# Optimization experiments

Measured on AMD Instinct MI355X. Metric: run time of the kernel, lower is better.

## Reference

```python
import jax, jax.numpy as jnp
import numpy as np

B, T, D = 1, 4096, 2048
NUM_HEADS, NUM_KV_HEADS, HEAD_DIM = 16, 8, 128
QUERY_PRE_ATTN_SCALAR = HEAD_DIM ** -0.5
SOFT_CAP = 50.0
WINDOW = 1024
ROPE_BASE = 10000.0
ROPE_SCALE = 1.0
K_MASK = -2.3819763e+38


def apply_rope(x, positions, head_dim, max_wavelength=ROPE_BASE, scale_factor=ROPE_SCALE):
    # x: [B, T, N, H], positions: [B, T]
    fraction = 2.0 * jnp.arange(head_dim // 2, dtype=jnp.float32) / head_dim
    timescale = max_wavelength ** fraction  # [H/2]
    sinusoid = positions[..., None].astype(jnp.float32) / timescale  # [B, T, H/2]
    sinusoid = (sinusoid / scale_factor)[..., None, :]  # [B, T, 1, H/2]
    sin, cos = jnp.sin(sinusoid), jnp.cos(sinusoid)
    first, second = jnp.split(x, 2, axis=-1)
    out = jnp.concatenate([first * cos - second * sin,
                           second * cos + first * sin], axis=-1)
    return out.astype(x.dtype)


def setup_inputs() -> dict:
    key = jax.random.key(0)
    ks = jax.random.split(key, 4)
    x = jax.random.normal(ks[0], (B, T, D), dtype=jnp.float32)
    segment_pos = jnp.broadcast_to(jnp.arange(T, dtype=jnp.int32), (B, T))
    # causal mask [B, T, S]
    attn_mask = jnp.broadcast_to(
        jnp.tril(jnp.ones((T, T), dtype=jnp.bool_)), (B, T, T))
    q_w = jax.random.normal(ks[1], (NUM_HEADS, D, HEAD_DIM), dtype=jnp.float32) * 0.02
    kv_w = jax.random.normal(ks[2], (2, NUM_KV_HEADS, D, HEAD_DIM), dtype=jnp.float32) * 0.02
    o_w = jax.random.normal(ks[3], (NUM_HEADS, HEAD_DIM, D), dtype=jnp.float32) * 0.02
    return {"x": x, "segment_pos": segment_pos, "attn_mask": attn_mask,
            "q_w": q_w, "kv_w": kv_w, "o_w": o_w}


def reference(x, segment_pos, attn_mask, q_w, kv_w, o_w):
    # Projections (GQA: separate q and kv einsums)
    q = jnp.einsum('BTD,NDH->BTNH', x, q_w)          # [B,T,N,H]
    k = jnp.einsum('BSD,KDH->BSKH', x, kv_w[0])      # [B,S,K,H]
    v = jnp.einsum('BSD,KDH->BSKH', x, kv_w[1])      # [B,S,K,H]

    q = apply_rope(q, segment_pos, HEAD_DIM)
    q = q * QUERY_PRE_ATTN_SCALAR
    k = apply_rope(k, segment_pos, HEAD_DIM)

    num_groups = NUM_HEADS // NUM_KV_HEADS
    qg = q.reshape(B, T, NUM_KV_HEADS, num_groups, HEAD_DIM)
    logits = jnp.einsum('BTKGH,BSKH->BTKGS', qg, k)
    logits = logits.reshape(B, T, NUM_HEADS, -1)     # [B,T,N,S]

    # soft cap
    logits = jnp.tanh(logits / SOFT_CAP) * SOFT_CAP

    # sliding-window mask combined with causal mask
    all_ones = jnp.ones_like(attn_mask)
    sliding = jnp.triu(all_ones, -WINDOW + 1) * jnp.tril(all_ones, WINDOW - 1)
    mask = sliding * attn_mask                       # [B,T,S] bool

    padded = jnp.where(mask[:, :, None, :], logits, K_MASK)
    probs = jax.nn.softmax(padded, axis=-1).astype(k.dtype)

    probs_g = probs.reshape(B, T, NUM_KV_HEADS, num_groups, -1)
    encoded = jnp.einsum('BTKGS,BSKH->BTKGH', probs_g, v)
    encoded = encoded.reshape(B, T, NUM_HEADS, HEAD_DIM)

    attn_output = jnp.einsum('BTNH,NHD->BTD', encoded, o_w)
    return attn_output
```

## Files before the change

kernel.cpp:

```cpp
#include <hip/hip_runtime.h>
#include <hip/hip_bf16.h>
#include <math.h>

typedef __attribute__((ext_vector_type(8))) short short8;
typedef __attribute__((ext_vector_type(8))) unsigned short ushort8;
typedef __attribute__((ext_vector_type(4))) float f32x4;

#define T_SEQ 4096
#define D_MODEL 2048
#define N_HEADS 16
#define N_KV 8
#define HEAD_DIM 128
#define QSCALE 0.08838834764831845f

__device__ __forceinline__ float bf2f(unsigned short u) {
  union { unsigned int i; float f; } x; x.i = ((unsigned int)u) << 16; return x.f;
}
__device__ __forceinline__ unsigned short f2bf(float f) {
  union { float f; unsigned int i; } x; x.f = f;
  unsigned int i = x.i;
  unsigned int r = i + 0x7fffu + ((i >> 16) & 1u);
  return (unsigned short)(r >> 16);
}

__global__ __launch_bounds__(256) void cvt_x_kernel(const float* __restrict__ x,
                                                    unsigned short* __restrict__ xb) {
  int idx = blockIdx.x * 256 + threadIdx.x;
  const float4* p = reinterpret_cast<const float4*>(x) + (size_t)idx * 2;
  float4 a = p[0], b = p[1];
  ushort8 o;
  o[0] = f2bf(a.x); o[1] = f2bf(a.y); o[2] = f2bf(a.z); o[3] = f2bf(a.w);
  o[4] = f2bf(b.x); o[5] = f2bf(b.y); o[6] = f2bf(b.z); o[7] = f2bf(b.w);
  reinterpret_cast<ushort8*>(xb)[idx] = o;
}

__global__ __launch_bounds__(256) void rope_table_kernel(const int* __restrict__ segpos,
                                                         float2* __restrict__ tab) {
  int idx = blockIdx.x * 256 + threadIdx.x;
  int t = idx >> 6, i = idx & 63;
  float pos = (float)segpos[t];
  float ts = powf(10000.f, (float)(2 * i) / 128.f);
  float ang = pos / ts;
  tab[idx] = make_float2(sinf(ang), cosf(ang));
}

__global__ __launch_bounds__(256) void transpose_f32_bf16_kernel(const float* __restrict__ src,
                                                                 unsigned short* __restrict__ dst,
                                                                 int sstride, int dstride,
                                                                 long sBatch, long dBatch) {
  __shared__ float tile[32][33];
  long b = blockIdx.z;
  src += b * sBatch; dst += b * dBatch;
  int c0 = blockIdx.x * 32, r0 = blockIdx.y * 32;
  int tx = threadIdx.x & 31, ty = threadIdx.x >> 5;
#pragma unroll
  for (int i = 0; i < 4; ++i)
    tile[ty + i * 8][tx] = src[(size_t)(r0 + ty + i * 8) * sstride + c0 + tx];
  __syncthreads();
#pragma unroll
  for (int i = 0; i < 4; ++i)
    dst[(size_t)(c0 + ty + i * 8) * dstride + r0 + tx] = f2bf(tile[tx][ty + i * 8]);
}

__global__ __launch_bounds__(256) void transpose_bf16_kernel(const unsigned short* __restrict__ src,
                                                             unsigned short* __restrict__ dst,
                                                             int sstride, int dstride,
                                                             long sBatch, long dBatch) {
  __shared__ unsigned short tile[32][33];
  long b = blockIdx.z;
  src += b * sBatch; dst += b * dBatch;
  int c0 = blockIdx.x * 32, r0 = blockIdx.y * 32;
  int tx = threadIdx.x & 31, ty = threadIdx.x >> 5;
#pragma unroll
  for (int i = 0; i < 4; ++i)
    tile[ty + i * 8][tx] = src[(size_t)(r0 + ty + i * 8) * sstride + c0 + tx];
  __syncthreads();
#pragma unroll
  for (int i = 0; i < 4; ++i)
    dst[(size_t)(c0 + ty + i * 8) * dstride + r0 + tx] = tile[tx][ty + i * 8];
}

#define G2L(gp, lp)                                                           \
  __builtin_amdgcn_global_load_lds(                                           \
      (const __attribute__((address_space(1))) void*)(gp),                    \
      (__attribute__((address_space(3))) void*)(lp), 16, 0, 0)
#define GBAR() asm volatile("s_barrier" ::: "memory")
#define VMW(n) asm volatile("s_waitcnt vmcnt(" #n ")" ::: "memory")

template <int OUT_BF16, int NHB>
__global__ __launch_bounds__(512, 2) void gemm256_kernel(const unsigned short* __restrict__ A,
                                                         const unsigned short* __restrict__ Bt,
                                                         void* __restrict__ Cout,
                                                         int M, int N, int K) {
  constexpr int NW = 2 * NHB;
  extern __shared__ unsigned short smem[];
  unsigned short* ldsA = smem;
  unsigned short* ldsB = smem + 32768;
  const int tid = threadIdx.x;
  const int lane = tid & 63, wave = tid >> 6;
  const int wm = wave >> 2, wn = wave & 3;
  const int lr = lane & 15, lg = lane >> 4;
  const int swz = (lr & 7) << 3;
  const int c0s = (lg * 8) ^ swz;
  const int c1s = (32 + lg * 8) ^ swz;

  int id = blockIdx.y * gridDim.x + blockIdx.x;
  int nb = gridDim.x * gridDim.y;
  int sw = (id & 7) * (nb >> 3) + (id >> 3);
  const long brow = (long)(sw / gridDim.x) * 256;
  const long bcol = (long)(sw % gridDim.x) * (128 * NHB);

  const unsigned short* Ag = A + brow * K;
  const unsigned short* Bg = Bt + bcol * K;

  const int r0 = tid >> 3;
  const int cs = ((tid & 7) * 8) ^ ((r0 & 7) << 3);

#define ST_A(tt, b, a)                                                        \
  { G2L(Ag + (size_t)((a) * 128 + r0) * K + (size_t)(tt) * 64 + cs,           \
        ldsA + (b) * 16384 + (a) * 8192 + tid * 8);                           \
    G2L(Ag + (size_t)((a) * 128 + r0 + 64) * K + (size_t)(tt) * 64 + cs,      \
        ldsA + (b) * 16384 + (a) * 8192 + 4096 + tid * 8); }
#define ST_B(tt, b, h)                                                        \
  { G2L(Bg + (size_t)((h) * 128 + r0) * K + (size_t)(tt) * 64 + cs,           \
        ldsB + (b) * 8192 * NHB + (h) * 8192 + tid * 8);                      \
    G2L(Bg + (size_t)((h) * 128 + r0 + 64) * K + (size_t)(tt) * 64 + cs,      \
        ldsB + (b) * 8192 * NHB + (h) * 8192 + 4096 + tid * 8); }

  f32x4 acc[8][NW] = {};
  short8 bf[NW][2];
  short8 af[4];

#define RD_B(b)                                                               \
  { const unsigned short* pb = ldsB + (b) * 8192 * NHB + wn * 2048 * NHB;     \
    _Pragma("unroll")                                                         \
    for (int n = 0; n < NW; ++n) {                                            \
      bf[n][0] = *(const short8*)(pb + (n * 16 + lr) * 64 + c0s);             \
      bf[n][1] = *(const short8*)(pb + (n * 16 + lr) * 64 + c1s);             \
    } }
#define RD_A(b, mb)                                                           \
  { const unsigned short* pa = ldsA + (b) * 16384 + wm * 8192;                \
    af[0] = *(const short8*)(pa + ((mb) * 16 + lr) * 64 + c0s);               \
    af[1] = *(const short8*)(pa + ((mb) * 16 + lr) * 64 + c1s);               \
    af[2] = *(const short8*)(pa + ((mb) * 16 + 16 + lr) * 64 + c0s);          \
    af[3] = *(const short8*)(pa + ((mb) * 16 + 16 + lr) * 64 + c1s); }
#define MFMA2(mb)                                                             \
  { __builtin_amdgcn_s_setprio(1);                                            \
    _Pragma("unroll")                                                         \
    for (int n = 0; n < NW; ++n) {                                            \
      acc[mb][n]     = __builtin_amdgcn_mfma_f32_16x16x32_bf16(af[0], bf[n][0], acc[mb][n], 0, 0, 0);     \
      acc[mb][n]     = __builtin_amdgcn_mfma_f32_16x16x32_bf16(af[1], bf[n][1], acc[mb][n], 0, 0, 0);     \
      acc[mb + 1][n] = __builtin_amdgcn_mfma_f32_16x16x32_bf16(af[2], bf[n][0], acc[mb + 1][n], 0, 0, 0); \
      acc[mb + 1][n] = __builtin_amdgcn_mfma_f32_16x16x32_bf16(af[3], bf[n][1], acc[mb + 1][n], 0, 0, 0); \
    }                                                                         \
    __builtin_amdgcn_s_setprio(0); }

  ST_B(0, 0, 0);
  if constexpr (NHB == 2) ST_B(0, 0, 1);
  ST_A(0, 0, 0); ST_A(0, 0, 1);
  ST_B(1, 1, 0);
  if constexpr (NHB == 2) ST_B(1, 1, 1);
  if constexpr (NHB == 2) { VMW(4); } else { VMW(2); }
  ST_A(1, 1, 0); ST_A(1, 1, 1);
  GBAR();

  const int NT = K >> 6;
  for (int j = 0; j < (NT >> 1); ++j) {
    const int t2 = 2 * j + 2, t3 = 2 * j + 3;
    const bool s2 = t2 < NT, s3 = t3 < NT;
    RD_B(0); RD_A(0, 0);
    if (s2) ST_B(t2, 0, 0);
    GBAR(); MFMA2(0); GBAR();
    RD_A(0, 2);
    if constexpr (NHB == 2) { if (s2) ST_B(t2, 0, 1); }
    GBAR(); MFMA2(2); GBAR();
    RD_A(0, 4);
    GBAR(); MFMA2(4); GBAR();
    RD_A(0, 6);
    if (s2) {
      if constexpr (NHB == 2) { VMW(4); } else { VMW(2); }
      ST_A(t2, 0, 0); ST_A(t2, 0, 1);
    } else { VMW(0); }
    GBAR(); MFMA2(6); GBAR();
    RD_B(1); RD_A(1, 0);
    if (s3) ST_B(t3, 1, 0);
    GBAR(); MFMA2(0); GBAR();
    RD_A(1, 2);
    if constexpr (NHB == 2) { if (s3) ST_B(t3, 1, 1); }
    GBAR(); MFMA2(2); GBAR();
    RD_A(1, 4);
    GBAR(); MFMA2(4); GBAR();
    RD_A(1, 6);
    if (s3) {
      if constexpr (NHB == 2) { VMW(4); } else { VMW(2); }
      ST_A(t3, 1, 0); ST_A(t3, 1, 1);
    } else { VMW(0); }
    GBAR(); MFMA2(6); GBAR();
  }

#undef ST_A
#undef ST_B
#undef RD_A
#undef RD_B
#undef MFMA2

#pragma unroll
  for (int m = 0; m < 8; ++m) {
#pragma unroll
    for (int i = 0; i < 4; ++i) {
      long row = brow + wm * 128 + m * 16 + lg * 4 + i;
#pragma unroll
      for (int n = 0; n < NW; ++n) {
        long col = bcol + wn * (32 * NHB) + n * 16 + lr;
        if (OUT_BF16)
          ((unsigned short*)Cout)[row * N + col] = f2bf(acc[m][n][i]);
        else
          ((float*)Cout)[row * N + col] = acc[m][n][i];
      }
    }
  }
}

__global__ __launch_bounds__(256) void rope_apply_kernel(const unsigned short* __restrict__ raw,
                                                         const float2* __restrict__ tab,
                                                         unsigned short* __restrict__ Qb,
                                                         unsigned short* __restrict__ Kb) {
  int gid = blockIdx.x * 256 + threadIdx.x;
  int j = gid & 7;
  int rem = gid >> 3;
  int hs = rem % 24;
  int t = rem / 24;
  int i0 = j * 8;
  float sv[8], cv[8];
  const float2* tp = tab + t * 64 + i0;
#pragma unroll
  for (int q = 0; q < 8; ++q) { float2 sc2 = tp[q]; sv[q] = sc2.x; cv[q] = sc2.y; }
  if (hs < 16) {
    const unsigned short* p = raw + (size_t)t * 4096 + hs * 128 + i0;
    ushort8 a = *(const ushort8*)p;
    ushort8 b = *(const ushort8*)(p + 64);
    ushort8 o1, o2;
#pragma unroll
    for (int q = 0; q < 8; ++q) {
      float fa = bf2f(a[q]), fb = bf2f(b[q]);
      o1[q] = f2bf((fa * cv[q] - fb * sv[q]) * QSCALE);
      o2[q] = f2bf((fb * cv[q] + fa * sv[q]) * QSCALE);
    }
    unsigned short* qp = Qb + ((size_t)hs * T_SEQ + t) * 128 + i0;
    *(ushort8*)qp = o1;
    *(ushort8*)(qp + 64) = o2;
  } else {
    int kn = hs - 16;
    const unsigned short* p = raw + (size_t)t * 4096 + 2048 + kn * 128 + i0;
    ushort8 a = *(const ushort8*)p;
    ushort8 b = *(const ushort8*)(p + 64);
    ushort8 o1, o2;
#pragma unroll
    for (int q = 0; q < 8; ++q) {
      float fa = bf2f(a[q]), fb = bf2f(b[q]);
      o1[q] = f2bf(fa * cv[q] - fb * sv[q]);
      o2[q] = f2bf(fb * cv[q] + fa * sv[q]);
    }
    unsigned short* kp = Kb + ((size_t)kn * T_SEQ + t) * 128 + i0;
    *(ushort8*)kp = o1;
    *(ushort8*)(kp + 64) = o2;
  }
}

__global__ __launch_bounds__(512) void attn_kernel(const unsigned short* __restrict__ Qb,
                                                   const unsigned short* __restrict__ Kb,
                                                   const unsigned short* __restrict__ Vt,
                                                   unsigned short* __restrict__ enc) {
  __shared__ unsigned short Ks[64][128];
  __shared__ unsigned short Vs[128][64];
  __shared__ unsigned short Ps[8][16][72];
  int lin = blockIdx.y * 32 + blockIdx.x;
  lin = (lin & 7) * 64 + (lin >> 3);
  const int h = lin >> 5;
  const int qb0 = (lin & 31) * 128;
  const int kvh = h >> 1;
  const int tid = threadIdx.x, lane = tid & 63, wave = tid >> 6;
  const int qw = qb0 + wave * 16;
  const int lr = lane & 15, lg = lane >> 4;
  const int sw = (lr & 7) << 3;

  short8 aq[4];
  {
    const unsigned short* qp = Qb + ((size_t)h * T_SEQ + qw + lr) * 128 + lg * 8;
#pragma unroll
    for (int c = 0; c < 4; ++c) aq[c] = *(const short8*)(qp + c * 32);
  }
  f32x4 acc[8] = {};
  float lsum = 0.f;

  const int s_lo = (qb0 - 1023) > 0 ? (qb0 - 1023) : 0;
  const int kb_lo = s_lo >> 6, kb_hi = (qb0 + 127) >> 6;

  const int rK = tid >> 4;
  const int cpK = (tid & 15) * 8;
  const int colK = cpK ^ ((rK & 7) << 3);
  const int rV = tid >> 3;
  const int cpV = (tid & 7) * 8;
  const int colV = cpV ^ ((rV & 7) << 3);
  const unsigned short* kgb = Kb + ((size_t)kvh * T_SEQ + rK) * 128 + colK;
  const unsigned short* vgb = Vt + ((size_t)kvh * 128 + rV) * T_SEQ + colV;

  ushort8 kr0, kr1, vr0, vr1;
  {
    const int s0g = kb_lo * 64;
    kr0 = *(const ushort8*)(kgb + (size_t)s0g * 128);
    kr1 = *(const ushort8*)(kgb + (size_t)(s0g + 32) * 128);
    vr0 = *(const ushort8*)(vgb + s0g);
    vr1 = *(const ushort8*)(vgb + (size_t)64 * T_SEQ + s0g);
  }

  const int qg = qw + lr;
  for (int kb = kb_lo; kb <= kb_hi; ++kb) {
    const int s0g = kb * 64;
    __syncthreads();
    *(ushort8*)&Ks[rK][cpK] = kr0;
    *(ushort8*)&Ks[rK + 32][cpK] = kr1;
    *(ushort8*)&Vs[rV][cpV] = vr0;
    *(ushort8*)&Vs[rV + 64][cpV] = vr1;
    __syncthreads();
    if (kb < kb_hi) {
      const int sn = s0g + 64;
      kr0 = *(const ushort8*)(kgb + (size_t)sn * 128);
      kr1 = *(const ushort8*)(kgb + (size_t)(sn + 32) * 128);
      vr0 = *(const ushort8*)(vgb + sn);
      vr1 = *(const ushort8*)(vgb + (size_t)64 * T_SEQ + sn);
    }
    if (s0g > qw + 15 || s0g + 63 < qw - 1023) continue;
    const bool interior = (s0g + 63 <= qw) && (s0g >= qw - 1008);

    f32x4 sT[4] = {};
#pragma unroll
    for (int st = 0; st < 4; ++st) {
      const int krow = st * 16 + lr;
#pragma unroll
      for (int c = 0; c < 4; ++c) {
        short8 kf = *(const short8*)&Ks[krow][(c * 32 + lg * 8) ^ sw];
        sT[st] = __builtin_amdgcn_mfma_f32_16x16x32_bf16(kf, aq[c], sT[st], 0, 0, 0);
      }
    }
#pragma unroll
    for (int st = 0; st < 4; ++st) {
      float p[4];
#pragma unroll
      for (int r = 0; r < 4; ++r) {
        float s = sT[st][r];
        float z2 = s * s * 4.0e-4f;
        float capped = s * (15.f + z2) * __builtin_amdgcn_rcpf(fmaf(z2, 6.f, 15.f));
        float pv = __expf(capped);
        if (!interior) {
          int sg = s0g + st * 16 + lg * 4 + r;
          pv = ((unsigned)(qg - sg) <= 1023u) ? pv : 0.f;
        }
        lsum += pv;
        p[r] = pv;
      }
      unsigned u0, u1;
      asm("v_cvt_pk_bf16_f32 %0, %1, %2" : "=v"(u0) : "v"(p[0]), "v"(p[1]));
      asm("v_cvt_pk_bf16_f32 %0, %1, %2" : "=v"(u1) : "v"(p[2]), "v"(p[3]));
      uint2 w; w.x = u0; w.y = u1;
      *(uint2*)&Ps[wave][lr][st * 16 + lg * 4] = w;
    }
    short8 pa0 = *(const short8*)&Ps[wave][lr][lg * 8];
    short8 pa1 = *(const short8*)&Ps[wave][lr][32 + lg * 8];
#pragma unroll
    for (int d0 = 0; d0 < 8; ++d0) {
      const int vrow = d0 * 16 + lr;
      short8 bv0 = *(const short8*)&Vs[vrow][(lg * 8) ^ sw];
      short8 bv1 = *(const short8*)&Vs[vrow][(32 + lg * 8) ^ sw];
      acc[d0] = __builtin_amdgcn_mfma_f32_16x16x32_bf16(pa0, bv0, acc[d0], 0, 0, 0);
      acc[d0] = __builtin_amdgcn_mfma_f32_16x16x32_bf16(pa1, bv1, acc[d0], 0, 0, 0);
    }
  }

  float l = lsum;
  l += __shfl_xor(l, 16);
  l += __shfl_xor(l, 32);
#pragma unroll
  for (int r = 0; r < 4; ++r) {
    float lt = __shfl(l, lg * 4 + r);
    float inv = __builtin_amdgcn_rcpf(lt);
    int row = qw + lg * 4 + r;
    unsigned short* op = enc + (size_t)row * D_MODEL + h * 128 + lr;
#pragma unroll
    for (int d0 = 0; d0 < 8; ++d0) op[d0 * 16] = f2bf(acc[d0][r] * inv);
  }
}

extern "C" void kernel_launch(void* const* d_in, const int* in_sizes, int n_in,
                              void* d_out, int out_size, void* d_ws, size_t ws_size,
                              hipStream_t stream) {
  const float* x = (const float*)d_in[0];
  const int* segpos = (const int*)d_in[1];
  const float* q_w = (const float*)d_in[3];
  const float* kv_w = (const float*)d_in[4];
  const float* o_w = (const float*)d_in[5];
  float* out = (float*)d_out;
  char* ws = (char*)d_ws;

  const size_t OFF_XB = 0;
  const size_t OFF_WT = OFF_XB + 16777216;
  const size_t OFF_RAW = OFF_WT + 16777216;
  const size_t OFF_KB = OFF_RAW + 33554432;
  const size_t OFF_VT = OFF_KB + 8388608;
  const size_t OFF_TAB = OFF_VT + 8388608;
  unsigned short* xb = (unsigned short*)(ws + OFF_XB);
  unsigned short* Wt = (unsigned short*)(ws + OFF_WT);
  unsigned short* raw = (unsigned short*)(ws + OFF_RAW);
  unsigned short* Kb = (unsigned short*)(ws + OFF_KB);
  unsigned short* Vt = (unsigned short*)(ws + OFF_VT);
  float2* tab = (float2*)(ws + OFF_TAB);
  unsigned short* o_wt = xb;
  unsigned short* Qb = Wt;
  unsigned short* enc = raw;

  hipFuncSetAttribute((const void*)(gemm256_kernel<1, 2>),
                      hipFuncAttributeMaxDynamicSharedMemorySize, 131072);
  hipFuncSetAttribute((const void*)(gemm256_kernel<0, 1>),
                      hipFuncAttributeMaxDynamicSharedMemorySize, 98304);

  cvt_x_kernel<<<dim3(4096), dim3(256), 0, stream>>>(x, xb);
  rope_table_kernel<<<dim3(1024), dim3(256), 0, stream>>>(segpos, tab);
  transpose_f32_bf16_kernel<<<dim3(4, 64, 16), dim3(256), 0, stream>>>(
      q_w, Wt, 128, 2048, (long)2048 * 128, (long)128 * 2048);
  transpose_f32_bf16_kernel<<<dim3(4, 64, 16), dim3(256), 0, stream>>>(
      kv_w, Wt + (size_t)2048 * 2048, 128, 2048, (long)2048 * 128, (long)128 * 2048);
  gemm256_kernel<1, 2><<<dim3(16, 16), dim3(512), 131072, stream>>>(xb, Wt, (void*)raw, 4096, 4096, 2048);
  transpose_f32_bf16_kernel<<<dim3(64, 64, 1), dim3(256), 0, stream>>>(
      o_w, o_wt, 2048, 2048, 0L, 0L);
  rope_apply_kernel<<<dim3(3072), dim3(256), 0, stream>>>(raw, tab, Qb, Kb);
  transpose_bf16_kernel<<<dim3(4, 128, 8), dim3(256), 0, stream>>>(
      raw + 3072, Vt, 4096, 4096, 128L, (long)128 * 4096);
  attn_kernel<<<dim3(32, 16), dim3(512), 0, stream>>>(Qb, Kb, Vt, enc);
  gemm256_kernel<0, 1><<<dim3(16, 16), dim3(512), 98304, stream>>>(enc, o_wt, (void*)out, 4096, 2048, 2048);
}
```

Before: 205.0 us.

## Merge prep kernels, shrink attention blocks to 64 queries, use exp2 and setprio

Several unrelated changes are bundled. The x conversion and rope-table kernels become one launch, the q/kv weight transposes become one launch, and rope application is fused with the V transpose, cutting the launch count. The attention kernel moves from 128-query, 8-wave blocks to 64-query, 4-wave blocks with 1024 blocks in total, and K/V register prefetch is adjusted to match. The softmax folds log2(e) into the soft-cap and masks with -inf before a raw v_exp_f32, and s_setprio is raised around the MFMA sections. Smaller blocks give more blocks per CU, but each block reloads K/V tiles shared across fewer queries, which increases K/V traffic.

```diff
diff --git a/kernel.cpp b/kernel.cpp
--- a/kernel.cpp
+++ b/kernel.cpp
@@ -23,61 +23,60 @@
   return (unsigned short)(r >> 16);
 }
 
-__global__ __launch_bounds__(256) void cvt_x_kernel(const float* __restrict__ x,
-                                                    unsigned short* __restrict__ xb) {
-  int idx = blockIdx.x * 256 + threadIdx.x;
-  const float4* p = reinterpret_cast<const float4*>(x) + (size_t)idx * 2;
-  float4 a = p[0], b = p[1];
-  ushort8 o;
-  o[0] = f2bf(a.x); o[1] = f2bf(a.y); o[2] = f2bf(a.z); o[3] = f2bf(a.w);
-  o[4] = f2bf(b.x); o[5] = f2bf(b.y); o[6] = f2bf(b.z); o[7] = f2bf(b.w);
-  reinterpret_cast<ushort8*>(xb)[idx] = o;
-}
-
-__global__ __launch_bounds__(256) void rope_table_kernel(const int* __restrict__ segpos,
-                                                         float2* __restrict__ tab) {
-  int idx = blockIdx.x * 256 + threadIdx.x;
-  int t = idx >> 6, i = idx & 63;
-  float pos = (float)segpos[t];
-  float ts = powf(10000.f, (float)(2 * i) / 128.f);
-  float ang = pos / ts;
-  tab[idx] = make_float2(sinf(ang), cosf(ang));
-}
-
-__global__ __launch_bounds__(256) void transpose_f32_bf16_kernel(const float* __restrict__ src,
-                                                                 unsigned short* __restrict__ dst,
-                                                                 int sstride, int dstride,
-                                                                 long sBatch, long dBatch) {
+__global__ __launch_bounds__(256) void prep_kernel(const float* __restrict__ x,
+                                                   unsigned short* __restrict__ xb,
+                                                   const int* __restrict__ segpos,
+                                                   float2* __restrict__ tab) {
+  int b = blockIdx.x;
+  if (b < 4096) {
+    int idx = b * 256 + threadIdx.x;
+    const float4* p = reinterpret_cast<const float4*>(x) + (size_t)idx * 2;
+    float4 a = p[0], c = p[1];
+    ushort8 o;
+    o[0] = f2bf(a.x); o[1] = f2bf(a.y); o[2] = f2bf(a.z); o[3] = f2bf(a.w);
+    o[4] = f2bf(c.x); o[5] = f2bf(c.y); o[6] = f2bf(c.z); o[7] = f2bf(c.w);
+    reinterpret_cast<ushort8*>(xb)[idx] = o;
+  } else {
+    int idx = (b - 4096) * 256 + threadIdx.x;
+    int t = idx >> 6, i = idx & 63;
+    float pos = (float)segpos[t];
+    float ts = powf(10000.f, (float)(2 * i) / 128.f);
+    float ang = pos / ts;
+    tab[idx] = make_float2(sinf(ang), cosf(ang));
+  }
+}
+
+__global__ __launch_bounds__(256) void wqkv_transpose_kernel(const float* __restrict__ q_w,
+                                                             const float* __restrict__ kv_w,
+                                                             unsigned short* __restrict__ Wt) {
   __shared__ float tile[32][33];
-  long b = blockIdx.z;
-  src += b * sBatch; dst += b * dBatch;
+  int z = blockIdx.z;
+  const float* src = (z < 16) ? q_w + (size_t)z * 2048 * 128
+                              : kv_w + (size_t)(z - 16) * 2048 * 128;
+  unsigned short* dst = Wt + (size_t)z * 128 * 2048;
   int c0 = blockIdx.x * 32, r0 = blockIdx.y * 32;
   int tx = threadIdx.x & 31, ty = threadIdx.x >> 5;
 #pragma unroll
   for (int i = 0; i < 4; ++i)
-    tile[ty + i * 8][tx] = src[(size_t)(r0 + ty + i * 8) * sstride + c0 + tx];
+    tile[ty + i * 8][tx] = src[(size_t)(r0 + ty + i * 8) * 128 + c0 + tx];
   __syncthreads();
 #pragma unroll
   for (int i = 0; i < 4; ++i)
-    dst[(size_t)(c0 + ty + i * 8) * dstride + r0 + tx] = f2bf(tile[tx][ty + i * 8]);
-}
-
-__global__ __launch_bounds__(256) void transpose_bf16_kernel(const unsigned short* __restrict__ src,
-                                                             unsigned short* __restrict__ dst,
-                                                             int sstride, int dstride,
-                                                             long sBatch, long dBatch) {
-  __shared__ unsigned short tile[32][33];
-  long b = blockIdx.z;
-  src += b * sBatch; dst += b * dBatch;
+    dst[(size_t)(c0 + ty + i * 8) * 2048 + r0 + tx] = f2bf(tile[tx][ty + i * 8]);
+}
+
+__global__ __launch_bounds__(256) void ow_transpose_kernel(const float* __restrict__ src,
+                                                           unsigned short* __restrict__ dst) {
+  __shared__ float tile[32][33];
   int c0 = blockIdx.x * 32, r0 = blockIdx.y * 32;
   int tx = threadIdx.x & 31, ty = threadIdx.x >> 5;
 #pragma unroll
   for (int i = 0; i < 4; ++i)
-    tile[ty + i * 8][tx] = src[(size_t)(r0 + ty + i * 8) * sstride + c0 + tx];
+    tile[ty + i * 8][tx] = src[(size_t)(r0 + ty + i * 8) * 2048 + c0 + tx];
   __syncthreads();
 #pragma unroll
   for (int i = 0; i < 4; ++i)
-    dst[(size_t)(c0 + ty + i * 8) * dstride + r0 + tx] = tile[tx][ty + i * 8];
+    dst[(size_t)(c0 + ty + i * 8) * 2048 + r0 + tx] = f2bf(tile[tx][ty + i * 8]);
 }
 
 #define G2L(gp, lp)                                                           \
@@ -221,63 +220,82 @@
   }
 }
 
-__global__ __launch_bounds__(256) void rope_apply_kernel(const unsigned short* __restrict__ raw,
-                                                         const float2* __restrict__ tab,
-                                                         unsigned short* __restrict__ Qb,
-                                                         unsigned short* __restrict__ Kb) {
-  int gid = blockIdx.x * 256 + threadIdx.x;
-  int j = gid & 7;
-  int rem = gid >> 3;
-  int hs = rem % 24;
-  int t = rem / 24;
-  int i0 = j * 8;
-  float sv[8], cv[8];
-  const float2* tp = tab + t * 64 + i0;
-#pragma unroll
-  for (int q = 0; q < 8; ++q) { float2 sc2 = tp[q]; sv[q] = sc2.x; cv[q] = sc2.y; }
-  if (hs < 16) {
-    const unsigned short* p = raw + (size_t)t * 4096 + hs * 128 + i0;
-    ushort8 a = *(const ushort8*)p;
-    ushort8 b = *(const ushort8*)(p + 64);
-    ushort8 o1, o2;
-#pragma unroll
-    for (int q = 0; q < 8; ++q) {
-      float fa = bf2f(a[q]), fb = bf2f(b[q]);
-      o1[q] = f2bf((fa * cv[q] - fb * sv[q]) * QSCALE);
-      o2[q] = f2bf((fb * cv[q] + fa * sv[q]) * QSCALE);
-    }
-    unsigned short* qp = Qb + ((size_t)hs * T_SEQ + t) * 128 + i0;
-    *(ushort8*)qp = o1;
-    *(ushort8*)(qp + 64) = o2;
+__global__ __launch_bounds__(256) void rope_vt_kernel(const unsigned short* __restrict__ raw,
+                                                      const float2* __restrict__ tab,
+                                                      unsigned short* __restrict__ Qb,
+                                                      unsigned short* __restrict__ Kb,
+                                                      unsigned short* __restrict__ Vt) {
+  __shared__ unsigned short tile[32][33];
+  int b = blockIdx.x;
+  if (b < 3072) {
+    int gid = b * 256 + threadIdx.x;
+    int j = gid & 7;
+    int rem = gid >> 3;
+    int hs = rem % 24;
+    int t = rem / 24;
+    int i0 = j * 8;
+    float sv[8], cv[8];
+    const float2* tp = tab + t * 64 + i0;
+#pragma unroll
+    for (int q = 0; q < 8; ++q) { float2 sc2 = tp[q]; sv[q] = sc2.x; cv[q] = sc2.y; }
+    if (hs < 16) {
+      const unsigned short* p = raw + (size_t)t * 4096 + hs * 128 + i0;
+      ushort8 a = *(const ushort8*)p;
+      ushort8 c = *(const ushort8*)(p + 64);
+      ushort8 o1, o2;
+#pragma unroll
+      for (int q = 0; q < 8; ++q) {
+        float fa = bf2f(a[q]), fb = bf2f(c[q]);
+        o1[q] = f2bf((fa * cv[q] - fb * sv[q]) * QSCALE);
+        o2[q] = f2bf((fb * cv[q] + fa * sv[q]) * QSCALE);
+      }
+      unsigned short* qp = Qb + ((size_t)hs * T_SEQ + t) * 128 + i0;
+      *(ushort8*)qp = o1;
+      *(ushort8*)(qp + 64) = o2;
+    } else {
+      int kn = hs - 16;
+      const unsigned short* p = raw + (size_t)t * 4096 + 2048 + kn * 128 + i0;
+      ushort8 a = *(const ushort8*)p;
+      ushort8 c = *(const ushort8*)(p + 64);
+      ushort8 o1, o2;
+#pragma unroll
+      for (int q = 0; q < 8; ++q) {
+        float fa = bf2f(a[q]), fb = bf2f(c[q]);
+        o1[q] = f2bf(fa * cv[q] - fb * sv[q]);
+        o2[q] = f2bf(fb * cv[q] + fa * sv[q]);
+      }
+      unsigned short* kp = Kb + ((size_t)kn * T_SEQ + t) * 128 + i0;
+      *(ushort8*)kp = o1;
+      *(ushort8*)(kp + 64) = o2;
+    }
   } else {
-    int kn = hs - 16;
-    const unsigned short* p = raw + (size_t)t * 4096 + 2048 + kn * 128 + i0;
-    ushort8 a = *(const ushort8*)p;
-    ushort8 b = *(const ushort8*)(p + 64);
-    ushort8 o1, o2;
-#pragma unroll
-    for (int q = 0; q < 8; ++q) {
-      float fa = bf2f(a[q]), fb = bf2f(b[q]);
-      o1[q] = f2bf(fa * cv[q] - fb * sv[q]);
-      o2[q] = f2bf(fb * cv[q] + fa * sv[q]);
-    }
-    unsigned short* kp = Kb + ((size_t)kn * T_SEQ + t) * 128 + i0;
-    *(ushort8*)kp = o1;
-    *(ushort8*)(kp + 64) = o2;
-  }
-}
-
-__global__ __launch_bounds__(512) void attn_kernel(const unsigned short* __restrict__ Qb,
-                                                   const unsigned short* __restrict__ Kb,
-                                                   const unsigned short* __restrict__ Vt,
-                                                   unsigned short* __restrict__ enc) {
+    int id = b - 3072;
+    int bx = id & 3, by = (id >> 2) & 127, bz = id >> 9;
+    const unsigned short* src = raw + 3072 + (size_t)bz * 128;
+    unsigned short* dst = Vt + (size_t)bz * 128 * 4096;
+    int c0 = bx * 32, r0 = by * 32;
+    int tx = threadIdx.x & 31, ty = threadIdx.x >> 5;
+#pragma unroll
+    for (int i = 0; i < 4; ++i)
+      tile[ty + i * 8][tx] = src[(size_t)(r0 + ty + i * 8) * 4096 + c0 + tx];
+    __syncthreads();
+#pragma unroll
+    for (int i = 0; i < 4; ++i)
+      dst[(size_t)(c0 + ty + i * 8) * 4096 + r0 + tx] = tile[tx][ty + i * 8];
+  }
+}
+
+__global__ __launch_bounds__(256, 4) void attn_kernel(const unsigned short* __restrict__ Qb,
+                                                      const unsigned short* __restrict__ Kb,
+                                                      const unsigned short* __restrict__ Vt,
+                                                      unsigned short* __restrict__ enc) {
   __shared__ unsigned short Ks[64][128];
   __shared__ unsigned short Vs[128][64];
-  __shared__ unsigned short Ps[8][16][72];
-  int lin = blockIdx.y * 32 + blockIdx.x;
-  lin = (lin & 7) * 64 + (lin >> 3);
-  const int h = lin >> 5;
-  const int qb0 = (lin & 31) * 128;
+  __shared__ unsigned short Ps[4][16][72];
+  int rawb = blockIdx.y * 64 + blockIdx.x;
+  int lin = (rawb & 7) * 128 + (rawb >> 3);
+  const int h = lin >> 6;
+  const int qb0 = (lin & 63) * 64;
   const int kvh = h >> 1;
   const int tid = threadIdx.x, lane = tid & 63, wave = tid >> 6;
   const int qw = qb0 + wave * 16;
@@ -294,7 +312,7 @@
   float lsum = 0.f;
 
   const int s_lo = (qb0 - 1023) > 0 ? (qb0 - 1023) : 0;
-  const int kb_lo = s_lo >> 6, kb_hi = (qb0 + 127) >> 6;
+  const int kb_lo = s_lo >> 6, kb_hi = (qb0 + 63) >> 6;
 
   const int rK = tid >> 4;
   const int cpK = (tid & 15) * 8;
@@ -305,35 +323,39 @@
   const unsigned short* kgb = Kb + ((size_t)kvh * T_SEQ + rK) * 128 + colK;
   const unsigned short* vgb = Vt + ((size_t)kvh * 128 + rV) * T_SEQ + colV;
 
-  ushort8 kr0, kr1, vr0, vr1;
+  ushort8 kr[4], vr[4];
   {
     const int s0g = kb_lo * 64;
-    kr0 = *(const ushort8*)(kgb + (size_t)s0g * 128);
-    kr1 = *(const ushort8*)(kgb + (size_t)(s0g + 32) * 128);
-    vr0 = *(const ushort8*)(vgb + s0g);
-    vr1 = *(const ushort8*)(vgb + (size_t)64 * T_SEQ + s0g);
+#pragma unroll
+    for (int j = 0; j < 4; ++j) {
+      kr[j] = *(const ushort8*)(kgb + (size_t)(s0g + j * 16) * 128);
+      vr[j] = *(const ushort8*)(vgb + (size_t)(j * 32) * T_SEQ + s0g);
+    }
   }
 
   const int qg = qw + lr;
   for (int kb = kb_lo; kb <= kb_hi; ++kb) {
     const int s0g = kb * 64;
     __syncthreads();
-    *(ushort8*)&Ks[rK][cpK] = kr0;
-    *(ushort8*)&Ks[rK + 32][cpK] = kr1;
-    *(ushort8*)&Vs[rV][cpV] = vr0;
-    *(ushort8*)&Vs[rV + 64][cpV] = vr1;
+#pragma unroll
+    for (int j = 0; j < 4; ++j) {
+      *(ushort8*)&Ks[rK + j * 16][cpK] = kr[j];
+      *(ushort8*)&Vs[rV + j * 32][cpV] = vr[j];
+    }
     __syncthreads();
     if (kb < kb_hi) {
       const int sn = s0g + 64;
-      kr0 = *(const ushort8*)(kgb + (size_t)sn * 128);
-      kr1 = *(const ushort8*)(kgb + (size_t)(sn + 32) * 128);
-      vr0 = *(const ushort8*)(vgb + sn);
-      vr1 = *(const ushort8*)(vgb + (size_t)64 * T_SEQ + sn);
+#pragma unroll
+      for (int j = 0; j < 4; ++j) {
+        kr[j] = *(const ushort8*)(kgb + (size_t)(sn + j * 16) * 128);
+        vr[j] = *(const ushort8*)(vgb + (size_t)(j * 32) * T_SEQ + sn);
+      }
     }
     if (s0g > qw + 15 || s0g + 63 < qw - 1023) continue;
     const bool interior = (s0g + 63 <= qw) && (s0g >= qw - 1008);
 
     f32x4 sT[4] = {};
+    __builtin_amdgcn_s_setprio(1);
 #pragma unroll
     for (int st = 0; st < 4; ++st) {
       const int krow = st * 16 + lr;
@@ -343,19 +365,22 @@
         sT[st] = __builtin_amdgcn_mfma_f32_16x16x32_bf16(kf, aq[c], sT[st], 0, 0, 0);
       }
     }
+    __builtin_amdgcn_s_setprio(0);
 #pragma unroll
     for (int st = 0; st < 4; ++st) {
       float p[4];
 #pragma unroll
       for (int r = 0; r < 4; ++r) {
         float s = sT[st][r];
+        float sl = s * 1.44269504f;
         float z2 = s * s * 4.0e-4f;
-        float capped = s * (15.f + z2) * __builtin_amdgcn_rcpf(fmaf(z2, 6.f, 15.f));
-        float pv = __expf(capped);
+        float e = sl * (15.f + z2) * __builtin_amdgcn_rcpf(fmaf(z2, 6.f, 15.f));
         if (!interior) {
           int sg = s0g + st * 16 + lg * 4 + r;
-          pv = ((unsigned)(qg - sg) <= 1023u) ? pv : 0.f;
+          e = ((unsigned)(qg - sg) <= 1023u) ? e : -__builtin_inff();
         }
+        float pv;
+        asm("v_exp_f32 %0, %1" : "=v"(pv) : "v"(e));
         lsum += pv;
         p[r] = pv;
       }
@@ -367,6 +392,7 @@
     }
     short8 pa0 = *(const short8*)&Ps[wave][lr][lg * 8];
     short8 pa1 = *(const short8*)&Ps[wave][lr][32 + lg * 8];
+    __builtin_amdgcn_s_setprio(1);
 #pragma unroll
     for (int d0 = 0; d0 < 8; ++d0) {
       const int vrow = d0 * 16 + lr;
@@ -375,6 +401,7 @@
       acc[d0] = __builtin_amdgcn_mfma_f32_16x16x32_bf16(pa0, bv0, acc[d0], 0, 0, 0);
       acc[d0] = __builtin_amdgcn_mfma_f32_16x16x32_bf16(pa1, bv1, acc[d0], 0, 0, 0);
     }
+    __builtin_amdgcn_s_setprio(0);
   }
 
   float l = lsum;
@@ -423,18 +450,11 @@
   hipFuncSetAttribute((const void*)(gemm256_kernel<0, 1>),
                       hipFuncAttributeMaxDynamicSharedMemorySize, 98304);
 
-  cvt_x_kernel<<<dim3(4096), dim3(256), 0, stream>>>(x, xb);
-  rope_table_kernel<<<dim3(1024), dim3(256), 0, stream>>>(segpos, tab);
-  transpose_f32_bf16_kernel<<<dim3(4, 64, 16), dim3(256), 0, stream>>>(
-      q_w, Wt, 128, 2048, (long)2048 * 128, (long)128 * 2048);
-  transpose_f32_bf16_kernel<<<dim3(4, 64, 16), dim3(256), 0, stream>>>(
-      kv_w, Wt + (size_t)2048 * 2048, 128, 2048, (long)2048 * 128, (long)128 * 2048);
+  prep_kernel<<<dim3(5120), dim3(256), 0, stream>>>(x, xb, segpos, tab);
+  wqkv_transpose_kernel<<<dim3(4, 64, 32), dim3(256), 0, stream>>>(q_w, kv_w, Wt);
   gemm256_kernel<1, 2><<<dim3(16, 16), dim3(512), 131072, stream>>>(xb, Wt, (void*)raw, 4096, 4096, 2048);
-  transpose_f32_bf16_kernel<<<dim3(64, 64, 1), dim3(256), 0, stream>>>(
-      o_w, o_wt, 2048, 2048, 0L, 0L);
-  rope_apply_kernel<<<dim3(3072), dim3(256), 0, stream>>>(raw, tab, Qb, Kb);
-  transpose_bf16_kernel<<<dim3(4, 128, 8), dim3(256), 0, stream>>>(
-      raw + 3072, Vt, 4096, 4096, 128L, (long)128 * 4096);
-  attn_kernel<<<dim3(32, 16), dim3(512), 0, stream>>>(Qb, Kb, Vt, enc);
+  ow_transpose_kernel<<<dim3(64, 64), dim3(256), 0, stream>>>(o_w, o_wt);
+  rope_vt_kernel<<<dim3(7168), dim3(256), 0, stream>>>(raw, tab, Qb, Kb, Vt);
+  attn_kernel<<<dim3(64, 16), dim3(256), 0, stream>>>(Qb, Kb, Vt, enc);
   gemm256_kernel<0, 1><<<dim3(16, 16), dim3(512), 98304, stream>>>(enc, o_wt, (void*)out, 4096, 2048, 2048);
 }
```

Result: slower. 211.9 us (+3.4%).
